# Performance work log

Hardware: AMD Instinct MI355X
Metric: run time of the kernel (lower is better)

Reference implementation:

```python
import jax, jax.numpy as jnp
import numpy as np

N = 50000
E = 800000
F_IN = 128
HID = 64
HEADS = 4
P = 16384


def setup_inputs() -> dict:
    key = jax.random.key(0)
    ks = jax.random.split(key, 20)
    s = 0.05
    inp = {
        'x': jax.random.normal(ks[0], (N, F_IN), jnp.float32),
        'edge_src': jax.random.randint(ks[1], (E,), 0, N, jnp.int32),
        'edge_dst': jax.random.randint(ks[2], (E,), 0, N, jnp.int32),
        'edge_attr': jax.random.uniform(ks[3], (E, 1), jnp.float32),
        'pair_indices': jax.random.randint(ks[4], (P, 2), 0, N, jnp.int32),
        # conv1: in=F_IN, heads=4, out=HID, edge_dim=1
        'W1': jax.random.normal(ks[5], (F_IN, HEADS * HID), jnp.float32) * s,
        'We1': jax.random.normal(ks[6], (1, HEADS * HID), jnp.float32) * s,
        'as1': jax.random.normal(ks[7], (HEADS, HID), jnp.float32) * s,
        'ad1': jax.random.normal(ks[8], (HEADS, HID), jnp.float32) * s,
        'ae1': jax.random.normal(ks[9], (HEADS, HID), jnp.float32) * s,
        'b1': jnp.zeros((HEADS * HID,), jnp.float32),
        # conv2: in=4*HID, heads=1, out=HID
        'W2': jax.random.normal(ks[10], (HEADS * HID, HID), jnp.float32) * s,
        'We2': jax.random.normal(ks[11], (1, HID), jnp.float32) * s,
        'as2': jax.random.normal(ks[12], (1, HID), jnp.float32) * s,
        'ad2': jax.random.normal(ks[13], (1, HID), jnp.float32) * s,
        'ae2': jax.random.normal(ks[14], (1, HID), jnp.float32) * s,
        'b2': jnp.zeros((HID,), jnp.float32),
        'Wlin': jax.random.normal(ks[15], (2 * HID, 1), jnp.float32) * s,
        'blin': jnp.zeros((1,), jnp.float32),
    }
    return inp


def gat_conv(x, src, dst, edge_attr, W, We, att_src, att_dst, att_edge, bias, heads, C):
    """PyG GATConv (add_self_loops=True, fill_value='mean', negative_slope=0.2, eval mode)."""
    n = x.shape[0]
    # self-loop edge_attr = mean of incoming edge attrs per node
    deg = jax.ops.segment_sum(jnp.ones_like(dst, dtype=edge_attr.dtype), dst, num_segments=n)
    loop_attr = jax.ops.segment_sum(edge_attr, dst, num_segments=n) / jnp.maximum(deg, 1.0)[:, None]
    loop = jnp.arange(n, dtype=src.dtype)
    src_f = jnp.concatenate([src, loop])
    dst_f = jnp.concatenate([dst, loop])
    ea = jnp.concatenate([edge_attr, loop_attr], axis=0)  # [E+N, 1]
    h = (x @ W).reshape(n, heads, C)                      # [N, H, C]
    a_src = (h * att_src).sum(-1)                         # [N, H]
    a_dst = (h * att_dst).sum(-1)
    e = (ea @ We).reshape(-1, heads, C)                   # [E+N, H, C]
    a_edge = (e * att_edge).sum(-1)                       # [E+N, H]
    alpha = jax.nn.leaky_relu(a_src[src_f] + a_dst[dst_f] + a_edge, 0.2)
    amax = jax.ops.segment_max(alpha, dst_f, num_segments=n)
    ex = jnp.exp(alpha - amax[dst_f])
    denom = jax.ops.segment_sum(ex, dst_f, num_segments=n)
    w = ex / denom[dst_f]                                 # segment softmax over dst
    msg = h[src_f] * w[..., None]                         # [E+N, H, C]
    out = jax.ops.segment_sum(msg, dst_f, num_segments=n) # [N, H, C]
    return out.reshape(n, heads * C) + bias


def reference(x, edge_src, edge_dst, edge_attr, pair_indices,
              W1, We1, as1, ad1, ae1, b1,
              W2, We2, as2, ad2, ae2, b2, Wlin, blin):
    # dropout is identity in eval mode
    h1 = jax.nn.elu(gat_conv(x, edge_src, edge_dst, edge_attr,
                             W1, We1, as1, ad1, ae1, b1, HEADS, HID))
    h2 = gat_conv(h1, edge_src, edge_dst, edge_attr,
                  W2, We2, as2, ad2, ae2, b2, 1, HID)
    d1 = h2[pair_indices[:, 0]]
    d2 = h2[pair_indices[:, 1]]
    pf = jnp.concatenate([d1, d2], axis=1)                # [P, 2*HID]
    return jax.nn.sigmoid(pf @ Wlin + blin).reshape(-1)
```

## Files before the change

kernel.cpp:

```cpp
#include <hip/hip_runtime.h>
#include <hip/hip_fp16.h>
#include <math.h>

typedef __attribute__((ext_vector_type(8))) short short8;
typedef __attribute__((ext_vector_type(4))) float floatx4;
typedef __attribute__((ext_vector_type(2))) float float2v;

#define LOG2E 1.4426950408889634f

__device__ __forceinline__ unsigned short f2bf(float f){
  unsigned int x = __float_as_uint(f);
  unsigned int r = x + 0x7fff + ((x >> 16) & 1);
  return (unsigned short)(r >> 16);
}
__device__ __forceinline__ unsigned char f2fp8(float v){
  int pk = __builtin_amdgcn_cvt_pk_fp8_f32(v, 0.f, 0, false);
  return (unsigned char)(pk & 0xff);
}
__device__ __forceinline__ float wsumf(float v){
#pragma unroll
  for (int o = 32; o; o >>= 1) v += __shfl_xor(v, o, 64);
  return v;
}
__device__ __forceinline__ unsigned pkh2(float a, float b){
  auto p = __builtin_amdgcn_cvt_pkrtz(a, b);
  unsigned u; __builtin_memcpy(&u, &p, 4); return u;
}
__device__ __forceinline__ float h2f(unsigned v){
  unsigned short us = (unsigned short)v;
  __fp16 h; __builtin_memcpy(&h, &us, 2);
  return (float)h;
}

__global__ __launch_bounds__(256) void k_count_prep(const int* __restrict__ dst,
    const float* __restrict__ eattr, unsigned* __restrict__ degp,
    unsigned char* __restrict__ rank, int E, int N, int ebl2,
    const float* __restrict__ W1, const float* __restrict__ as1,
    const float* __restrict__ ad1, const float* __restrict__ W2,
    const float* __restrict__ as2, const float* __restrict__ ad2,
    const float* __restrict__ We1, const float* __restrict__ ae1,
    const float* __restrict__ We2, const float* __restrict__ ae2,
    const float* __restrict__ b2, const float* __restrict__ Wlin,
    unsigned short* __restrict__ W1p, float* __restrict__ w2vT,
    float* __restrict__ ce){
  if ((int)blockIdx.x < ebl2){
    int e0 = blockIdx.x * 512 + threadIdx.x;
    int e1 = e0 + 256;
    bool v0 = e0 < E, v1 = e1 < E;
    int d0 = 0, d1 = 0; float a0 = 0.f, a1 = 0.f;
    if (v0){ d0 = dst[e0]; a0 = eattr[e0]; }
    if (v1){ d1 = dst[e1]; a1 = eattr[e1]; }
    int b0 = (e0 >> 8) & 7, b1 = (e1 >> 8) & 7;
    if (v0){
      unsigned old = atomicAdd(&degp[(size_t)b0 * N + d0],
                               (1u << 24) | (unsigned)(a0 * 262144.0f));
      rank[e0] = (unsigned char)(old >> 24);
    }
    if (v1){
      unsigned old = atomicAdd(&degp[(size_t)b1 * N + d1],
                               (1u << 24) | (unsigned)(a1 * 262144.0f));
      rank[e1] = (unsigned char)(old >> 24);
    }
    return;
  }
  if (threadIdx.x >= 64) return;
  int b = blockIdx.x - ebl2, lane = threadIdx.x;
  if (b < 68){
    int nt = b >> 2, kc = b & 3;
    int col = lane & 15, krow = kc * 32 + (lane >> 4) * 8;
    unsigned short tmp[8];
    if (nt < 16){
#pragma unroll
      for (int j = 0; j < 8; j++) tmp[j] = f2bf(W1[(size_t)(krow + j) * 256 + nt * 16 + col]);
    } else {
#pragma unroll
      for (int j = 0; j < 8; j++){
        float v = 0.f;
        if (col < 8){
          const float* av = (col < 4) ? as1 : ad1;
          int h = col & 3;
          for (int c = 0; c < 64; c++)
            v += W1[(size_t)(krow + j) * 256 + h * 64 + c] * av[h * 64 + c];
          v *= LOG2E;
        }
        tmp[j] = f2bf(v);
      }
    }
    unsigned short* dstp = W1p + (((size_t)nt * 4 + kc) * 64 + lane) * 8;
    *(ushort4*)(dstp)     = make_ushort4(tmp[0], tmp[1], tmp[2], tmp[3]);
    *(ushort4*)(dstp + 4) = make_ushort4(tmp[4], tmp[5], tmp[6], tmp[7]);
  } else if (b < 72){
    int k = (b - 68) * 64 + lane;
    float4 a = make_float4(0.f, 0.f, 0.f, 0.f);
    for (int c = 0; c < 64; c++){
      float wv = W2[(size_t)k * 64 + c];
      a.x += wv * as2[c];
      a.y += wv * ad2[c];
      a.z += wv * Wlin[c];
      a.w += wv * Wlin[64 + c];
    }
    w2vT[k]       = a.x * LOG2E;
    w2vT[256 + k] = a.y * LOG2E;
    w2vT[512 + k] = a.z;
    w2vT[768 + k] = a.w;
  } else {
    float p0 = We1[lane]       * ae1[lane];
    float p1 = We1[64 + lane]  * ae1[64 + lane];
    float p2 = We1[128 + lane] * ae1[128 + lane];
    float p3 = We1[192 + lane] * ae1[192 + lane];
    float p4 = We2[lane]       * ae2[lane];
    float c1 = b2[lane] * Wlin[lane];
    float c2 = b2[lane] * Wlin[64 + lane];
    p0 = wsumf(p0); p1 = wsumf(p1); p2 = wsumf(p2); p3 = wsumf(p3); p4 = wsumf(p4);
    c1 = wsumf(c1); c2 = wsumf(c2);
    if (lane == 0){
      ce[0] = p0 * LOG2E; ce[1] = p1 * LOG2E; ce[2] = p2 * LOG2E; ce[3] = p3 * LOG2E;
      ce[4] = p4 * LOG2E;
      ce[5] = c1; ce[6] = c2;
    }
  }
}

__global__ __launch_bounds__(256) void k_scan1_gemm(
    const unsigned* __restrict__ degp, int* __restrict__ row_ptr,
    int* __restrict__ bsum, int n, int gbl,
    const float* __restrict__ A, const unsigned short* __restrict__ Bp,
    unsigned char* __restrict__ h1f8, float* __restrict__ asrc,
    float* __restrict__ adst, int M){
  __shared__ unsigned short Bs[256 * 128];
  if ((int)blockIdx.x >= gbl){
    int* sm = (int*)Bs;
    int sb = blockIdx.x - gbl;
    int tid = threadIdx.x, gid = sb * 256 + tid;
    int v = 0;
    if (gid < n){
#pragma unroll
      for (int b = 0; b < 8; b++) v += (int)(degp[(size_t)b * n + gid] >> 24);
    }
    sm[tid] = v; __syncthreads();
    int pin = 0;
    for (int off = 1; off < 256; off <<= 1){
      int t = sm[pin * 256 + tid];
      if (tid >= off) t += sm[pin * 256 + tid - off];
      sm[(pin ^ 1) * 256 + tid] = t; pin ^= 1; __syncthreads();
    }
    int incl = sm[pin * 256 + tid];
    if (gid < n) row_ptr[gid] = incl - v;
    if (tid == 255) bsum[sb] = incl;
    return;
  }
  constexpr int K = 128, NKC = 4;
  {
    const uint4* srcp = (const uint4*)Bp;
    uint4* dstp = (uint4*)Bs;
    for (int i = threadIdx.x; i < 4096; i += 256) dstp[i] = srcp[i];
  }
  __syncthreads();
  int wave = threadIdx.x >> 6, lane = threadIdx.x & 63;
  int quad = lane >> 4, col = lane & 15;
  int r0 = (blockIdx.x * 4 + wave) * 16;
  int rowc = min(r0 + col, M - 1);
  short8 af[NKC], sf[NKC];
#pragma unroll
  for (int kc = 0; kc < NKC; kc++){
    float4 a0 = *(const float4*)(A + (size_t)rowc * K + kc * 32 + quad * 8);
    float4 a1 = *(const float4*)(A + (size_t)rowc * K + kc * 32 + quad * 8 + 4);
    short8 t;
    t[0] = (short)f2bf(a0.x); t[1] = (short)f2bf(a0.y);
    t[2] = (short)f2bf(a0.z); t[3] = (short)f2bf(a0.w);
    t[4] = (short)f2bf(a1.x); t[5] = (short)f2bf(a1.y);
    t[6] = (short)f2bf(a1.z); t[7] = (short)f2bf(a1.w);
    af[kc] = t;
    sf[kc] = *(const short8*)(Bp + (((size_t)16 * 4 + kc) * 64 + lane) * 8);
  }
  floatx4 acc[17];
#pragma unroll
  for (int nt = 0; nt < 17; nt++) acc[nt] = (floatx4){0.f, 0.f, 0.f, 0.f};
#pragma unroll
  for (int kc = 0; kc < NKC; kc++){
#pragma unroll
    for (int nt = 0; nt < 16; nt++){
      short8 bfv = *(const short8*)(&Bs[((nt * NKC + kc) * 64 + lane) * 8]);
      acc[nt] = __builtin_amdgcn_mfma_f32_16x16x32_bf16(af[kc], bfv, acc[nt], 0, 0, 0);
    }
    acc[16] = __builtin_amdgcn_mfma_f32_16x16x32_bf16(af[kc], sf[kc], acc[16], 0, 0, 0);
  }
#pragma unroll
  for (int nt = 0; nt < 16; nt++){
#pragma unroll
    for (int i = 0; i < 4; i++){
      int r = r0 + quad * 4 + i;
      if (r < M) h1f8[(size_t)r * 256 + nt * 16 + col] = f2fp8(acc[nt][i]);
    }
  }
#pragma unroll
  for (int i = 0; i < 4; i++){
    int r = r0 + quad * 4 + i;
    if (r < M){
      float v = acc[16][i];
      if (col < 4)      asrc[(size_t)r * 4 + col] = v;
      else if (col < 8) adst[(size_t)r * 4 + (col - 4)] = v;
    }
  }
}

__global__ __launch_bounds__(256) void k_scan3(int* __restrict__ row_ptr,
    const int* __restrict__ bsum, const unsigned* __restrict__ degp,
    float* __restrict__ lattr, int* __restrict__ base, int n, int E){
  int tid = threadIdx.x;
  int partial = (tid < (int)blockIdx.x) ? bsum[tid] : 0;
#pragma unroll
  for (int o = 32; o; o >>= 1) partial += __shfl_xor(partial, o, 64);
  __shared__ int ws[4];
  if ((tid & 63) == 0) ws[tid >> 6] = partial;
  __syncthreads();
  int blockOfs = ws[0] + ws[1] + ws[2] + ws[3];
  int gid = blockIdx.x * 256 + tid;
  if (gid >= n) return;
  int rp = row_ptr[gid] + blockOfs;
  row_ptr[gid] = rp;
  int cum = 0; float s = 0.f;
  int bb[8];
#pragma unroll
  for (int b = 0; b < 8; b++){
    unsigned p = degp[(size_t)b * n + gid];
    bb[b] = rp + cum;
    cum += (int)(p >> 24);
    s += (float)(p & 0xffffffu);
  }
  lattr[gid] = (s * (1.0f / 262144.0f)) / fmaxf((float)cum, 1.0f);
  int4* bp = (int4*)(base + (size_t)gid * 8);
  bp[0] = make_int4(bb[0], bb[1], bb[2], bb[3]);
  bp[1] = make_int4(bb[4], bb[5], bb[6], bb[7]);
  if (gid == 0) row_ptr[n] = E;
}

__global__ __launch_bounds__(256) void k_scatter(const int* __restrict__ src,
    const int* __restrict__ dst, const float* __restrict__ eattr,
    const unsigned char* __restrict__ rank, const int* __restrict__ base,
    const float* __restrict__ a_src, int4* __restrict__ csr, int E){
  int e0 = blockIdx.x * 512 + threadIdx.x;
  int e1 = e0 + 256;
  bool v0 = e0 < E, v1 = e1 < E;
  int b0 = (e0 >> 8) & 7, b1 = (e1 >> 8) & 7;
  if (v0){
    int d = dst[e0], s = src[e0];
    int pos = base[(size_t)d * 8 + b0] + (int)rank[e0];
    float4 av = *(const float4*)(a_src + ((size_t)s << 2));
    csr[pos] = make_int4(s, __float_as_int(eattr[e0]),
                         (int)pkh2(av.x, av.y), (int)pkh2(av.z, av.w));
  }
  if (v1){
    int d = dst[e1], s = src[e1];
    int pos = base[(size_t)d * 8 + b1] + (int)rank[e1];
    float4 av = *(const float4*)(a_src + ((size_t)s << 2));
    csr[pos] = make_int4(s, __float_as_int(eattr[e1]),
                         (int)pkh2(av.x, av.y), (int)pkh2(av.z, av.w));
  }
}

__global__ __launch_bounds__(256) void k_gat1(
    const int* __restrict__ row_ptr, const int4* __restrict__ csr,
    const float* __restrict__ lattr,
    const float* __restrict__ a_src, const float* __restrict__ a_dst,
    const float* __restrict__ ce, const unsigned char* __restrict__ hpre,
    const float* __restrict__ bias, const float* __restrict__ w2vT,
    float4* __restrict__ upd, int n){
  int node = blockIdx.x * 4 + (threadIdx.x >> 6);
  if (node >= n) return;
  int lane = threadIdx.x & 63;
  int q = lane >> 4, lsub = lane & 15, hq = lsub >> 2;
  int start = row_ptr[node], deg = row_ptr[node + 1] - start;
  float4 as4 = *(const float4*)(a_src + (size_t)node * 4);
  float4 ad4 = *(const float4*)(a_dst + (size_t)node * 4);
  float4 ce4 = *(const float4*)ce;
  float la = lattr[node];
  float asvh = hq == 0 ? as4.x : hq == 1 ? as4.y : hq == 2 ? as4.z : as4.w;
  float advh = hq == 0 ? ad4.x : hq == 1 ? ad4.y : hq == 2 ? ad4.z : ad4.w;
  float ceh  = hq == 0 ? ce4.x : hq == 1 ? ce4.y : hq == 2 ? ce4.z : ce4.w;
  unsigned lso = (unsigned)(lsub << 4);
  int hsh = (hq & 1) * 16;
  float2v acc2[8];
#pragma unroll
  for (int k = 0; k < 8; k++) acc2[k] = (float2v){0.f, 0.f};
  float dn = 0.f;
  if (q == 0){
    float aself = fmaf(la, ceh, asvh + advh);
    aself = aself > 0.f ? aself : 0.2f * aself;
    float wself = __builtin_amdgcn_exp2f(aself);
    dn = wself;
    uint4 u = *(const uint4*)(hpre + (((unsigned)node << 8) + lso));
    float2v w2 = (float2v){wself, wself};
    unsigned uu[4] = {u.x, u.y, u.z, u.w};
#pragma unroll
    for (int j = 0; j < 4; j++){
      acc2[2 * j]     = w2 * __builtin_amdgcn_cvt_pk_f32_fp8((int)uu[j], false);
      acc2[2 * j + 1] = w2 * __builtin_amdgcn_cvt_pk_f32_fp8((int)uu[j], true);
    }
  }
  for (int e = q; e < deg; e += 8){
    bool vB = (e + 4) < deg;
    int4 sA = csr[start + e];
    int4 sB = csr[start + (vB ? e + 4 : e)];
    uint4 uA = *(const uint4*)(hpre + (((unsigned)sA.x << 8) + lso));
    uint4 uB = *(const uint4*)(hpre + (((unsigned)sB.x << 8) + lso));
    unsigned hwA = (hq & 2) ? (unsigned)sA.w : (unsigned)sA.z;
    unsigned hwB = (hq & 2) ? (unsigned)sB.w : (unsigned)sB.z;
    float gA = h2f(hwA >> hsh);
    float gB = h2f(hwB >> hsh);
    float aA = fmaf(__int_as_float(sA.y), ceh, gA + advh);
    float aB = fmaf(__int_as_float(sB.y), ceh, gB + advh);
    aA = aA > 0.f ? aA : 0.2f * aA;
    aB = aB > 0.f ? aB : 0.2f * aB;
    float wA = __builtin_amdgcn_exp2f(aA);
    float wB = vB ? __builtin_amdgcn_exp2f(aB) : 0.f;
    dn += wA + wB;
    float2v wA2 = (float2v){wA, wA}, wB2 = (float2v){wB, wB};
    unsigned ua[4] = {uA.x, uA.y, uA.z, uA.w};
    unsigned ub[4] = {uB.x, uB.y, uB.z, uB.w};
#pragma unroll
    for (int j = 0; j < 4; j++){
      acc2[2 * j]     += wA2 * __builtin_amdgcn_cvt_pk_f32_fp8((int)ua[j], false);
      acc2[2 * j + 1] += wA2 * __builtin_amdgcn_cvt_pk_f32_fp8((int)ua[j], true);
      acc2[2 * j]     += wB2 * __builtin_amdgcn_cvt_pk_f32_fp8((int)ub[j], false);
      acc2[2 * j + 1] += wB2 * __builtin_amdgcn_cvt_pk_f32_fp8((int)ub[j], true);
    }
  }
  dn += __shfl_xor(dn, 16, 64);
  dn += __shfl_xor(dn, 32, 64);
#pragma unroll
  for (int k = 0; k < 8; k++){
    acc2[k].x += __shfl_xor(acc2[k].x, 16, 64);
    acc2[k].x += __shfl_xor(acc2[k].x, 32, 64);
    acc2[k].y += __shfl_xor(acc2[k].y, 16, 64);
    acc2[k].y += __shfl_xor(acc2[k].y, 32, 64);
  }
  {
    float inv = 1.f / dn;
    float d = 0.f;
#pragma unroll
    for (int j = 0; j < 4; j++){
      float4 b4  = *(const float4*)(bias + lsub * 16 + j * 4);
      float4 wvj = *(const float4*)(w2vT + (size_t)lane * 16 + j * 4);
      float bbv[4] = {b4.x, b4.y, b4.z, b4.w};
      float wvv[4] = {wvj.x, wvj.y, wvj.z, wvj.w};
#pragma unroll
      for (int t = 0; t < 4; t++){
        int k = j * 4 + t;
        float av = (k & 1) ? acc2[k >> 1].y : acc2[k >> 1].x;
        float v = av * inv + bbv[t];
        v = v > 0.f ? v : (__expf(v) - 1.f);
        d += v * wvv[t];
      }
    }
#pragma unroll
    for (int o = 1; o < 16; o <<= 1) d += __shfl_xor(d, o, 64);
    if (lsub == 0) ((float*)&upd[node])[q] = d;
  }
}

__global__ __launch_bounds__(256) void k_gat2(
    const int* __restrict__ row_ptr, const int4* __restrict__ csr,
    const float* __restrict__ lattr, const float4* __restrict__ upd,
    const float* __restrict__ ce,
    float* __restrict__ s1v, float* __restrict__ s2v, int n){
  int node = blockIdx.x * 32 + (threadIdx.x >> 3);
  if (node >= n) return;
  int lane8 = threadIdx.x & 7;
  int start = row_ptr[node], deg = row_ptr[node + 1] - start;
  float4 own = upd[node];
  float ad = own.y, c = ce[4];
  const float* updf = (const float*)upd;
  float t1 = 0.f, t2 = 0.f, dn = 0.f;
  if (lane8 == 0){
    float a = fmaf(lattr[node], c, own.x + ad);
    a = a > 0.f ? a : 0.2f * a;
    float w = __builtin_amdgcn_exp2f(a);
    dn = w; t1 = w * own.z; t2 = w * own.w;
  }
  for (int e = lane8; e < deg; e += 16){
    bool vB = (e + 8) < deg;
    int4 sA = csr[start + e];
    int4 sB = csr[start + (vB ? e + 8 : e)];
    float4 oA = *(const float4*)(updf + ((unsigned)sA.x << 2));
    float4 oB = *(const float4*)(updf + ((unsigned)sB.x << 2));
    float aA = fmaf(__int_as_float(sA.y), c, oA.x + ad);
    float aB = fmaf(__int_as_float(sB.y), c, oB.x + ad);
    aA = aA > 0.f ? aA : 0.2f * aA;
    aB = aB > 0.f ? aB : 0.2f * aB;
    float wA = __builtin_amdgcn_exp2f(aA);
    float wB = vB ? __builtin_amdgcn_exp2f(aB) : 0.f;
    dn += wA + wB;
    t1 = fmaf(wA, oA.z, fmaf(wB, oB.z, t1));
    t2 = fmaf(wA, oA.w, fmaf(wB, oB.w, t2));
  }
#pragma unroll
  for (int o = 1; o < 8; o <<= 1){
    dn += __shfl_xor(dn, o, 64);
    t1 += __shfl_xor(t1, o, 64);
    t2 += __shfl_xor(t2, o, 64);
  }
  if (lane8 == 0){
    float inv = 1.f / dn;
    s1v[node] = t1 * inv + ce[5];
    s2v[node] = t2 * inv + ce[6];
  }
}

__global__ __launch_bounds__(256) void k_pairs(const int* __restrict__ pairs,
    const float* __restrict__ s1v, const float* __restrict__ s2v,
    const float* __restrict__ blin, float* __restrict__ out, int P){
  int p = blockIdx.x * 256 + threadIdx.x;
  if (p >= P) return;
  int i = pairs[2 * p], j = pairs[2 * p + 1];
  float x = s1v[i] + s2v[j] + blin[0];
  out[p] = 1.f / (1.f + __expf(-x));
}

extern "C" void kernel_launch(void* const* d_in, const int* in_sizes, int n_in,
                              void* d_out, int out_size, void* d_ws, size_t ws_size,
                              hipStream_t stream) {
  const float* x     = (const float*)d_in[0];
  const int*   esrc  = (const int*)  d_in[1];
  const int*   edst  = (const int*)  d_in[2];
  const float* eattr = (const float*)d_in[3];
  const int*   pairs = (const int*)  d_in[4];
  const float* W1    = (const float*)d_in[5];
  const float* We1   = (const float*)d_in[6];
  const float* as1   = (const float*)d_in[7];
  const float* ad1   = (const float*)d_in[8];
  const float* ae1   = (const float*)d_in[9];
  const float* b1    = (const float*)d_in[10];
  const float* W2    = (const float*)d_in[11];
  const float* We2   = (const float*)d_in[12];
  const float* as2   = (const float*)d_in[13];
  const float* ad2   = (const float*)d_in[14];
  const float* ae2   = (const float*)d_in[15];
  const float* b2    = (const float*)d_in[16];
  const float* Wlin  = (const float*)d_in[17];
  const float* blin  = (const float*)d_in[18];
  float* out = (float*)d_out;

  const int N = in_sizes[0] / 128;
  const int E = in_sizes[1];
  const int P = in_sizes[4] / 2;

  char* w = (char*)d_ws;
  size_t off = 0;
  auto alloc = [&](size_t bytes) -> size_t {
    size_t r = off; off = (off + bytes + 255) & ~(size_t)255; return r;
  };
  size_t o_degp   = alloc((size_t)N * 32);
  size_t zero_end = off;
  size_t o_rank   = alloc((size_t)E);
  size_t o_rowptr = alloc((size_t)(N + 1) * 4);
  size_t o_bsum   = alloc(1024);
  size_t o_lattr  = alloc((size_t)N * 4);
  size_t o_base   = alloc((size_t)N * 32);
  size_t o_csr    = alloc((size_t)E * 16);
  size_t o_asrc1  = alloc((size_t)N * 16);
  size_t o_adst1  = alloc((size_t)N * 16);
  size_t o_upd    = alloc((size_t)N * 16);
  size_t o_ce     = alloc(64);
  size_t o_s1     = alloc((size_t)N * 4);
  size_t o_s2     = alloc((size_t)N * 4);
  size_t o_W1p    = alloc((size_t)17 * 4 * 64 * 8 * 2);
  size_t o_w2v    = alloc(256 * 16);
  size_t o_h1f8   = alloc((size_t)N * 256);
  (void)ws_size;

  unsigned* degp = (unsigned*)(w + o_degp);
  unsigned char* rank = (unsigned char*)(w + o_rank);
  int*   rowptr = (int*)  (w + o_rowptr);
  int*   bsum   = (int*)  (w + o_bsum);
  float* lattr  = (float*)(w + o_lattr);
  int*   base   = (int*)  (w + o_base);
  int4*  csr    = (int4*) (w + o_csr);
  float* asrc1  = (float*)(w + o_asrc1);
  float* adst1  = (float*)(w + o_adst1);
  float4* upd   = (float4*)(w + o_upd);
  float* ce     = (float*)(w + o_ce);
  float* s1v    = (float*)(w + o_s1);
  float* s2v    = (float*)(w + o_s2);
  unsigned short* W1p = (unsigned short*)(w + o_W1p);
  float* w2vT   = (float*)(w + o_w2v);
  unsigned char* h1f8 = (unsigned char*)(w + o_h1f8);

  (void)hipMemsetAsync(w, 0, zero_end, stream);

  int ebl2 = (E + 511) / 512;
  int nbl = (N + 255) / 256;
  int gbl = (N + 63) / 64;
  int wbl = (N + 3) / 4;

  k_count_prep<<<ebl2 + 73, 256, 0, stream>>>(edst, eattr, degp, rank, E, N, ebl2,
      W1, as1, ad1, W2, as2, ad2, We1, ae1, We2, ae2, b2, Wlin, W1p, w2vT, ce);
  k_scan1_gemm<<<gbl + nbl, 256, 0, stream>>>(degp, rowptr, bsum, N, gbl,
      x, W1p, h1f8, asrc1, adst1, N);
  k_scan3<<<nbl, 256, 0, stream>>>(rowptr, bsum, degp, lattr, base, N, E);
  k_scatter<<<ebl2, 256, 0, stream>>>(esrc, edst, eattr, rank, base, asrc1, csr, E);
  k_gat1<<<wbl, 256, 0, stream>>>(rowptr, csr, lattr, asrc1, adst1, ce,
                                  h1f8, b1, w2vT, upd, N);
  k_gat2<<<(N + 31) / 32, 256, 0, stream>>>(rowptr, csr, lattr, upd, ce,
                                            s1v, s2v, N);
  k_pairs<<<(P + 255) / 256, 256, 0, stream>>>(pairs, s1v, s2v, blin, out, P);
}
```

Measured before the change: 250.1 us.

## Double GEMM rows per wave, use hardware bf16 pack, shrink GAT blocks

The fused scan/GEMM kernel now has each wave compute two 16-row tiles, so every B fragment read from LDS feeds two MFMAs and the one-time LDS fill of W1 is spread over twice as many rows. The float-to-bf16 conversion now uses the packed v_cvt_pk_bf16_f32 instruction instead of software rounding. The two GAT aggregation kernels switch from 256-thread to 128-thread blocks for finer scheduling granularity. In exchange, the GEMM kernel holds twice as many accumulator registers, which may limit occupancy, and it launches half as many GEMM blocks.

```diff
diff --git a/kernel.cpp b/kernel.cpp
--- a/kernel.cpp
+++ b/kernel.cpp
@@ -12,6 +12,17 @@
   unsigned int x = __float_as_uint(f);
   unsigned int r = x + 0x7fff + ((x >> 16) & 1);
   return (unsigned short)(r >> 16);
+}
+__device__ __forceinline__ unsigned cvtpkbf(float lo, float hi){
+  unsigned r;
+  asm("v_cvt_pk_bf16_f32 %0, %1, %2" : "=v"(r) : "v"(lo), "v"(hi));
+  return r;
+}
+__device__ __forceinline__ short8 pk8(float4 a0, float4 a1){
+  unsigned t[4];
+  t[0] = cvtpkbf(a0.x, a0.y); t[1] = cvtpkbf(a0.z, a0.w);
+  t[2] = cvtpkbf(a1.x, a1.y); t[3] = cvtpkbf(a1.z, a1.w);
+  short8 r; __builtin_memcpy(&r, t, 16); return r;
 }
 __device__ __forceinline__ unsigned char f2fp8(float v){
   int pk = __builtin_amdgcn_cvt_pk_fp8_f32(v, 0.f, 0, false);
@@ -121,7 +132,7 @@
   }
 }
 
-__global__ __launch_bounds__(256) void k_scan1_gemm(
+__global__ __launch_bounds__(256, 2) void k_scan1_gemm(
     const unsigned* __restrict__ degp, int* __restrict__ row_ptr,
     int* __restrict__ bsum, int n, int gbl,
     const float* __restrict__ A, const unsigned short* __restrict__ Bp,
@@ -158,46 +169,68 @@
   __syncthreads();
   int wave = threadIdx.x >> 6, lane = threadIdx.x & 63;
   int quad = lane >> 4, col = lane & 15;
-  int r0 = (blockIdx.x * 4 + wave) * 16;
-  int rowc = min(r0 + col, M - 1);
-  short8 af[NKC], sf[NKC];
+  int r0a = blockIdx.x * 128 + wave * 16;
+  int r0b = r0a + 64;
+  int rowa = min(r0a + col, M - 1);
+  int rowb = min(r0b + col, M - 1);
+  short8 afa[NKC], afb[NKC], sf[NKC];
 #pragma unroll
   for (int kc = 0; kc < NKC; kc++){
-    float4 a0 = *(const float4*)(A + (size_t)rowc * K + kc * 32 + quad * 8);
-    float4 a1 = *(const float4*)(A + (size_t)rowc * K + kc * 32 + quad * 8 + 4);
-    short8 t;
-    t[0] = (short)f2bf(a0.x); t[1] = (short)f2bf(a0.y);
-    t[2] = (short)f2bf(a0.z); t[3] = (short)f2bf(a0.w);
-    t[4] = (short)f2bf(a1.x); t[5] = (short)f2bf(a1.y);
-    t[6] = (short)f2bf(a1.z); t[7] = (short)f2bf(a1.w);
-    af[kc] = t;
+    float4 a0 = *(const float4*)(A + (size_t)rowa * K + kc * 32 + quad * 8);
+    float4 a1 = *(const float4*)(A + (size_t)rowa * K + kc * 32 + quad * 8 + 4);
+    float4 b0 = *(const float4*)(A + (size_t)rowb * K + kc * 32 + quad * 8);
+    float4 b1 = *(const float4*)(A + (size_t)rowb * K + kc * 32 + quad * 8 + 4);
+    afa[kc] = pk8(a0, a1);
+    afb[kc] = pk8(b0, b1);
     sf[kc] = *(const short8*)(Bp + (((size_t)16 * 4 + kc) * 64 + lane) * 8);
   }
-  floatx4 acc[17];
-#pragma unroll
-  for (int nt = 0; nt < 17; nt++) acc[nt] = (floatx4){0.f, 0.f, 0.f, 0.f};
+  floatx4 acc0[17], acc1[17];
+#pragma unroll
+  for (int nt = 0; nt < 17; nt++){
+    acc0[nt] = (floatx4){0.f, 0.f, 0.f, 0.f};
+    acc1[nt] = (floatx4){0.f, 0.f, 0.f, 0.f};
+  }
 #pragma unroll
   for (int kc = 0; kc < NKC; kc++){
 #pragma unroll
     for (int nt = 0; nt < 16; nt++){
       short8 bfv = *(const short8*)(&Bs[((nt * NKC + kc) * 64 + lane) * 8]);
-      acc[nt] = __builtin_amdgcn_mfma_f32_16x16x32_bf16(af[kc], bfv, acc[nt], 0, 0, 0);
-    }
-    acc[16] = __builtin_amdgcn_mfma_f32_16x16x32_bf16(af[kc], sf[kc], acc[16], 0, 0, 0);
+      acc0[nt] = __builtin_amdgcn_mfma_f32_16x16x32_bf16(afa[kc], bfv, acc0[nt], 0, 0, 0);
+      acc1[nt] = __builtin_amdgcn_mfma_f32_16x16x32_bf16(afb[kc], bfv, acc1[nt], 0, 0, 0);
+    }
+    acc0[16] = __builtin_amdgcn_mfma_f32_16x16x32_bf16(afa[kc], sf[kc], acc0[16], 0, 0, 0);
+    acc1[16] = __builtin_amdgcn_mfma_f32_16x16x32_bf16(afb[kc], sf[kc], acc1[16], 0, 0, 0);
   }
 #pragma unroll
   for (int nt = 0; nt < 16; nt++){
 #pragma unroll
     for (int i = 0; i < 4; i++){
-      int r = r0 + quad * 4 + i;
-      if (r < M) h1f8[(size_t)r * 256 + nt * 16 + col] = f2fp8(acc[nt][i]);
+      int r = r0a + quad * 4 + i;
+      if (r < M) h1f8[(size_t)r * 256 + nt * 16 + col] = f2fp8(acc0[nt][i]);
     }
   }
 #pragma unroll
   for (int i = 0; i < 4; i++){
-    int r = r0 + quad * 4 + i;
+    int r = r0a + quad * 4 + i;
     if (r < M){
-      float v = acc[16][i];
+      float v = acc0[16][i];
+      if (col < 4)      asrc[(size_t)r * 4 + col] = v;
+      else if (col < 8) adst[(size_t)r * 4 + (col - 4)] = v;
+    }
+  }
+#pragma unroll
+  for (int nt = 0; nt < 16; nt++){
+#pragma unroll
+    for (int i = 0; i < 4; i++){
+      int r = r0b + quad * 4 + i;
+      if (r < M) h1f8[(size_t)r * 256 + nt * 16 + col] = f2fp8(acc1[nt][i]);
+    }
+  }
+#pragma unroll
+  for (int i = 0; i < 4; i++){
+    int r = r0b + quad * 4 + i;
+    if (r < M){
+      float v = acc1[16][i];
       if (col < 4)      asrc[(size_t)r * 4 + col] = v;
       else if (col < 8) adst[(size_t)r * 4 + (col - 4)] = v;
     }
@@ -259,14 +292,14 @@
   }
 }
 
-__global__ __launch_bounds__(256) void k_gat1(
+__global__ __launch_bounds__(128) void k_gat1(
     const int* __restrict__ row_ptr, const int4* __restrict__ csr,
     const float* __restrict__ lattr,
     const float* __restrict__ a_src, const float* __restrict__ a_dst,
     const float* __restrict__ ce, const unsigned char* __restrict__ hpre,
     const float* __restrict__ bias, const float* __restrict__ w2vT,
     float4* __restrict__ upd, int n){
-  int node = blockIdx.x * 4 + (threadIdx.x >> 6);
+  int node = blockIdx.x * 2 + (threadIdx.x >> 6);
   if (node >= n) return;
   int lane = threadIdx.x & 63;
   int q = lane >> 4, lsub = lane & 15, hq = lsub >> 2;
@@ -359,12 +392,12 @@
   }
 }
 
-__global__ __launch_bounds__(256) void k_gat2(
+__global__ __launch_bounds__(128) void k_gat2(
     const int* __restrict__ row_ptr, const int4* __restrict__ csr,
     const float* __restrict__ lattr, const float4* __restrict__ upd,
     const float* __restrict__ ce,
     float* __restrict__ s1v, float* __restrict__ s2v, int n){
-  int node = blockIdx.x * 32 + (threadIdx.x >> 3);
+  int node = blockIdx.x * 16 + (threadIdx.x >> 3);
   if (node >= n) return;
   int lane8 = threadIdx.x & 7;
   int start = row_ptr[node], deg = row_ptr[node + 1] - start;
@@ -490,8 +523,8 @@
 
   int ebl2 = (E + 511) / 512;
   int nbl = (N + 255) / 256;
-  int gbl = (N + 63) / 64;
-  int wbl = (N + 3) / 4;
+  int gbl = (N + 127) / 128;
+  int wbl = (N + 1) / 2;
 
   k_count_prep<<<ebl2 + 73, 256, 0, stream>>>(edst, eattr, degp, rank, E, N, ebl2,
       W1, as1, ad1, W2, as2, ad2, We1, ae1, We2, ae2, b2, Wlin, W1p, w2vT, ce);
@@ -499,9 +532,9 @@
       x, W1p, h1f8, asrc1, adst1, N);
   k_scan3<<<nbl, 256, 0, stream>>>(rowptr, bsum, degp, lattr, base, N, E);
   k_scatter<<<ebl2, 256, 0, stream>>>(esrc, edst, eattr, rank, base, asrc1, csr, E);
-  k_gat1<<<wbl, 256, 0, stream>>>(rowptr, csr, lattr, asrc1, adst1, ce,
+  k_gat1<<<wbl, 128, 0, stream>>>(rowptr, csr, lattr, asrc1, adst1, ce,
                                   h1f8, b1, w2vT, upd, N);
-  k_gat2<<<(N + 31) / 32, 256, 0, stream>>>(rowptr, csr, lattr, upd, ce,
+  k_gat2<<<(N + 15) / 16, 128, 0, stream>>>(rowptr, csr, lattr, upd, ce,
                                             s1v, s2v, N);
   k_pairs<<<(P + 255) / 256, 256, 0, stream>>>(pairs, s1v, s2v, blin, out, P);
 }
```

Result: no change. 247.5 us (-1.0%).
